# Kernel optimization log

Measured on AMD Instinct MI355X. Metric: run time of the kernel, lower is better.

## Reference

```python
import jax, jax.numpy as jnp
import numpy as np

D_MODEL = 1024
N_HEADS = 16
HEAD_DIM = D_MODEL // N_HEADS
WINDOW = 256


def setup_inputs() -> dict:
    key = jax.random.key(0)
    kx, kq, ko = jax.random.split(key, 3)
    B, T = 4, 2048
    x = jax.random.normal(kx, (B, T, D_MODEL), dtype=jnp.float32)
    s = 1.0 / np.sqrt(D_MODEL)
    w_qkv = jax.random.normal(kq, (D_MODEL, 3 * D_MODEL), dtype=jnp.float32) * s
    w_out = jax.random.normal(ko, (D_MODEL, D_MODEL), dtype=jnp.float32) * s
    return {"x": x, "w_qkv": w_qkv, "w_out": w_out}


def reference(x, w_qkv, w_out):
    B, T, C = x.shape
    qkv = (x @ w_qkv).reshape(B, T, 3, N_HEADS, HEAD_DIM)
    q, k, v = qkv[:, :, 0], qkv[:, :, 1], qkv[:, :, 2]  # [B,T,H,D]
    # sliding-window causal mask: position i attends to j in (i-W, i]
    i = jnp.arange(T)[:, None]
    j = jnp.arange(T)[None, :]
    allowed = (j <= i) & (j > i - WINDOW)
    mask = jnp.where(allowed, 0.0, -jnp.inf).astype(x.dtype)  # [T,T]
    scale = 1.0 / np.sqrt(HEAD_DIM)
    scores = jnp.einsum('bqhd,bkhd->bhqk', q, k) * scale + mask
    attn = jax.nn.softmax(scores, axis=-1)
    out = jnp.einsum('bhqk,bkhd->bqhd', attn, v).reshape(B, T, C)
    return out @ w_out
```

## Files before the change

### kernel.cpp

```cpp
#include <hip/hip_runtime.h>

typedef unsigned short u16;
typedef __attribute__((ext_vector_type(8))) short bh8;
typedef __attribute__((ext_vector_type(4))) float f4;
typedef __attribute__((ext_vector_type(4))) unsigned short us4;

#define T_SEQ 2048
#define NHEADS 16
#define DHEAD 64
#define WIN 256

__device__ __forceinline__ float bf2f(u16 u) {
  union { unsigned int i; float f; } v; v.i = ((unsigned int)u) << 16; return v.f;
}
__device__ __forceinline__ u16 f2bf(float f) {
  unsigned int u = __float_as_uint(f);
  u = u + 0x7fffu + ((u >> 16) & 1u);
  return (u16)(u >> 16);
}
__device__ __forceinline__ void async16(const void* g, void* l) {
  void* gv = const_cast<void*>(g);
  __builtin_amdgcn_global_load_lds(
      (__attribute__((address_space(1))) void*)gv,
      (__attribute__((address_space(3))) void*)l, 16, 0, 0);
}

__global__ void detect_dtype(const void* x, int* flag) {
  if (threadIdx.x == 0 && blockIdx.x == 0) {
    const float* xf = (const float*)x;
    int ok = 1;
    for (int i = 0; i < 128; ++i) {
      float v = xf[i];
      float a = fabsf(v);
      if (!(a < 64.f)) { ok = 0; break; }
      if (!(v == 0.f || a > 1e-30f)) { ok = 0; break; }
    }
    *flag = ok;
  }
}

__global__ __launch_bounds__(256) void prep(
    const void* __restrict__ x, const void* __restrict__ w_qkv,
    const void* __restrict__ w_out, u16* __restrict__ xbf,
    u16* __restrict__ wqkvT, u16* __restrict__ woutT,
    const int* __restrict__ flag, int have_x)
{
  const int bid = blockIdx.x;
  const int tid = threadIdx.x;
  const int isf = *flag;

  if (bid < 4096) {
    if (!have_x) return;
    const size_t e = ((size_t)bid * 256 + tid) * 8;
    if (isf) {
      const float* f = (const float*)x;
      us4 o0, o1;
      #pragma unroll
      for (int u = 0; u < 4; ++u) { o0[u] = f2bf(f[e + u]); o1[u] = f2bf(f[e + 4 + u]); }
      *(us4*)&xbf[e] = o0; *(us4*)&xbf[e + 4] = o1;
    } else {
      *(us4*)&xbf[e]     = *(const us4*)&((const u16*)x)[e];
      *(us4*)&xbf[e + 4] = *(const us4*)&((const u16*)x)[e + 4];
    }
  } else {
    __shared__ alignas(16) u16 tile[32][33];
    const void* in; u16* out; int C, bx, by;
    if (bid < 4096 + 3072) { const int t = bid - 4096; in = w_qkv; out = wqkvT; C = 3072; bx = t % 96; by = t / 96; }
    else                   { const int t = bid - 7168; in = w_out; out = woutT; C = 1024; bx = t % 32; by = t / 32; }
    const int R = 1024;
    const int tx = tid & 31, ty = tid >> 5;
    const int xg = bx * 32 + tx;
    const int y0 = by * 32;
    #pragma unroll
    for (int i = ty; i < 32; i += 8) {
      u16 v;
      if (isf) v = f2bf(((const float*)in)[(size_t)(y0 + i) * C + xg]);
      else     v = ((const u16*)in)[(size_t)(y0 + i) * C + xg];
      tile[i][tx] = v;
    }
    __syncthreads();
    const int ox  = y0 + tx;
    const int oy0 = bx * 32;
    #pragma unroll
    for (int i = ty; i < 32; i += 8)
      out[(size_t)(oy0 + i) * R + ox] = tile[tx][i];
  }
}

template<bool ADYN, bool CDYN>
__global__ __launch_bounds__(256, 4) void gemm_bt(
    const void* __restrict__ A, const u16* __restrict__ Bt,
    void* __restrict__ C, int N, int K, int lda, int ldc,
    const int* __restrict__ flag)
{
  __shared__ alignas(16) u16 As[128 * 64];
  __shared__ alignas(16) u16 Bs[128 * 64];

  const int isf  = ADYN ? *flag : 0;
  const int tid  = threadIdx.x;
  const int lane = tid & 63;
  const int w    = tid >> 6;
  const int wm   = (w >> 1) * 64;
  const int wn   = (w & 1) * 64;
  const int quad = lane >> 4;
  const int l16  = lane & 15;
  const int row0 = blockIdx.y * 128;
  const int col0 = blockIdx.x * 128;

  f4 acc[4][4] = {};

  size_t aoff[4]; const u16* bsrc[4]; int lofs[4];
  #pragma unroll
  for (int s = 0; s < 4; ++s) {
    const int r  = s * 32 + (tid >> 3);
    const int gc = (tid & 7) ^ (r & 7);
    aoff[s] = (size_t)(row0 + r) * lda + gc * 8;
    bsrc[s] = Bt + (size_t)(col0 + r) * K + gc * 8;
    lofs[s] = s * 4096 + tid * 16;
  }

  const bool af32 = ADYN && isf;

  for (int k0 = 0; k0 < K; k0 += 64) {
    if (af32) {
      const float* Af = (const float*)A;
      bh8 a[4];
      #pragma unroll
      for (int s = 0; s < 4; ++s) {
        f4 u0 = *(const f4*)(Af + aoff[s] + k0);
        f4 u1 = *(const f4*)(Af + aoff[s] + k0 + 4);
        #pragma unroll
        for (int u = 0; u < 4; ++u) { a[s][u] = (short)f2bf(u0[u]); a[s][u + 4] = (short)f2bf(u1[u]); }
      }
      __syncthreads();
      #pragma unroll
      for (int s = 0; s < 4; ++s) {
        *(bh8*)((char*)As + lofs[s]) = a[s];
        async16(bsrc[s] + k0, (char*)Bs + lofs[s]);
      }
    } else {
      const u16* A16 = (const u16*)A;
      __syncthreads();
      #pragma unroll
      for (int s = 0; s < 4; ++s) {
        async16(A16 + aoff[s] + k0, (char*)As + lofs[s]);
        async16(bsrc[s] + k0,       (char*)Bs + lofs[s]);
      }
    }
    __builtin_amdgcn_s_waitcnt(0);
    __syncthreads();

    #pragma unroll
    for (int ks = 0; ks < 2; ++ks) {
      bh8 af[4], bf[4];
      #pragma unroll
      for (int i = 0; i < 4; ++i) {
        const int row = wm + i * 16 + l16;
        const int lc  = (ks * 4 + quad) ^ (row & 7);
        af[i] = *(const bh8*)(As + row * 64 + lc * 8);
      }
      #pragma unroll
      for (int j = 0; j < 4; ++j) {
        const int row = wn + j * 16 + l16;
        const int lc  = (ks * 4 + quad) ^ (row & 7);
        bf[j] = *(const bh8*)(Bs + row * 64 + lc * 8);
      }
      #pragma unroll
      for (int i = 0; i < 4; ++i)
        #pragma unroll
        for (int j = 0; j < 4; ++j)
          acc[i][j] = __builtin_amdgcn_mfma_f32_16x16x32_bf16(af[i], bf[j], acc[i][j], 0, 0, 0);
    }
  }

  const bool cf32 = CDYN && (*flag);
  #pragma unroll
  for (int i = 0; i < 4; ++i) {
    #pragma unroll
    for (int j = 0; j < 4; ++j) {
      const int rb = row0 + wm + i * 16 + quad * 4;
      const int cc = col0 + wn + j * 16 + l16;
      #pragma unroll
      for (int r = 0; r < 4; ++r) {
        if (cf32) ((float*)C)[(size_t)(rb + r) * ldc + cc] = acc[i][j][r];
        else      ((u16*)C)[(size_t)(rb + r) * ldc + cc]   = f2bf(acc[i][j][r]);
      }
    }
  }
}

__global__ __launch_bounds__(256) void attn_mfma(u16* __restrict__ qkv)
{
  __shared__ alignas(16) u16 Qs[64 * 72];
  __shared__ alignas(16) u16 Kt[64 * 72];
  __shared__ alignas(16) u16 Vt[64 * 72];
  __shared__ alignas(16) u16 Ps[64 * 72];

  const int tid  = threadIdx.x;
  const int lane = tid & 63;
  const int w    = tid >> 6;
  const int quad = lane >> 4;
  const int l16  = lane & 15;
  const int qb = blockIdx.x, h = blockIdx.y, b = blockIdx.z;
  const int qs = qb * 64;

  const u16* base = qkv + (size_t)b * T_SEQ * 3072 + h * 64;

  const int c8  = (tid & 7) * 8;
  const int r0s = tid >> 3;
  #pragma unroll
  for (int r = r0s; r < 64; r += 32)
    *(bh8*)&Qs[r * 72 + c8] = *(const bh8*)&base[(size_t)(qs + r) * 3072 + c8];

  f4 Oc[4] = {};
  float mst[4] = {-1e30f, -1e30f, -1e30f, -1e30f};
  float lst[4] = {0.f, 0.f, 0.f, 0.f};

  const int tmin = (qb >= 4) ? 0 : (4 - qb);

  for (int t = tmin; t < 5; ++t) {
    const int kt0 = qs - 256 + t * 64;
    __syncthreads();

    #pragma unroll
    for (int r = r0s; r < 64; r += 32) {
      *(bh8*)&Kt[r * 72 + c8] =
          *(const bh8*)&base[(size_t)(kt0 + r) * 3072 + 1024 + c8];
      bh8 v = *(const bh8*)&base[(size_t)(kt0 + r) * 3072 + 2048 + c8];
      const int kc = r >> 3, ki = r & 7;
      #pragma unroll
      for (int u = 0; u < 8; ++u) {
        const int d = c8 + u;
        Vt[d * 72 + ((kc ^ (d >> 3)) << 3) + ki] = (u16)v[u];
      }
    }
    __syncthreads();

    const int qrow = (w * 16 + l16) * 72;
    bh8 qa0 = *(const bh8*)&Qs[qrow + quad * 8];
    bh8 qa1 = *(const bh8*)&Qs[qrow + 32 + quad * 8];
    f4 S[4];
    #pragma unroll
    for (int kb = 0; kb < 4; ++kb) {
      const int krow = (kb * 16 + l16) * 72;
      bh8 kf0 = *(const bh8*)&Kt[krow + quad * 8];
      bh8 kf1 = *(const bh8*)&Kt[krow + 32 + quad * 8];
      f4 s = {};
      s = __builtin_amdgcn_mfma_f32_16x16x32_bf16(qa0, kf0, s, 0, 0, 0);
      s = __builtin_amdgcn_mfma_f32_16x16x32_bf16(qa1, kf1, s, 0, 0, 0);
      S[kb] = s;
    }

    const int iq0 = qs + w * 16 + quad * 4;
    float tmax[4] = {-1e30f, -1e30f, -1e30f, -1e30f};
    #pragma unroll
    for (int kb = 0; kb < 4; ++kb) {
      const int j = kt0 + kb * 16 + l16;
      #pragma unroll
      for (int rr = 0; rr < 4; ++rr) {
        const int i = iq0 + rr;
        float s = S[kb][rr] * 0.125f;
        const bool ok = (j <= i) && (j > i - WIN);
        s = ok ? s : -1e30f;
        S[kb][rr] = s;
        tmax[rr] = fmaxf(tmax[rr], s);
      }
    }
    #pragma unroll
    for (int off = 1; off < 16; off <<= 1)
      #pragma unroll
      for (int rr = 0; rr < 4; ++rr)
        tmax[rr] = fmaxf(tmax[rr], __shfl_xor(tmax[rr], off));

    float alpha[4], rsum[4];
    #pragma unroll
    for (int rr = 0; rr < 4; ++rr) {
      const float mnew = fmaxf(mst[rr], tmax[rr]);
      alpha[rr] = __expf(mst[rr] - mnew);
      mst[rr] = mnew;
      rsum[rr] = 0.f;
    }

    const int swq = quad >> 1;
    #pragma unroll
    for (int kb = 0; kb < 4; ++kb) {
      const int kc = kb * 2 + (l16 >> 3);
      const int ki = l16 & 7;
      #pragma unroll
      for (int rr = 0; rr < 4; ++rr) {
        const float sv = S[kb][rr];
        const float p = (sv > -0.5e30f) ? __expf(sv - mst[rr]) : 0.f;
        rsum[rr] += p;
        const int q = w * 16 + quad * 4 + rr;
        Ps[q * 72 + ((kc ^ swq) << 3) + ki] = f2bf(p);
      }
    }
    #pragma unroll
    for (int off = 1; off < 16; off <<= 1)
      #pragma unroll
      for (int rr = 0; rr < 4; ++rr)
        rsum[rr] += __shfl_xor(rsum[rr], off);
    #pragma unroll
    for (int rr = 0; rr < 4; ++rr)
      lst[rr] = lst[rr] * alpha[rr] + rsum[rr];

    #pragma unroll
    for (int db = 0; db < 4; ++db)
      #pragma unroll
      for (int rr = 0; rr < 4; ++rr)
        Oc[db][rr] *= alpha[rr];

    {
      const int q = w * 16 + l16;
      const int sw = (q >> 3) & 1;
      bh8 pa0 = *(const bh8*)&Ps[q * 72 + (((0 + quad) ^ sw) << 3)];
      bh8 pa1 = *(const bh8*)&Ps[q * 72 + (((4 + quad) ^ sw) << 3)];
      #pragma unroll
      for (int db = 0; db < 4; ++db) {
        const int d = db * 16 + l16;
        const int dsw = d >> 3;
        bh8 vb0 = *(const bh8*)&Vt[d * 72 + (((0 + quad) ^ dsw) << 3)];
        bh8 vb1 = *(const bh8*)&Vt[d * 72 + (((4 + quad) ^ dsw) << 3)];
        Oc[db] = __builtin_amdgcn_mfma_f32_16x16x32_bf16(pa0, vb0, Oc[db], 0, 0, 0);
        Oc[db] = __builtin_amdgcn_mfma_f32_16x16x32_bf16(pa1, vb1, Oc[db], 0, 0, 0);
      }
    }
  }

  u16* obase = (u16*)base;
  #pragma unroll
  for (int rr = 0; rr < 4; ++rr) {
    const int i = qs + w * 16 + quad * 4 + rr;
    const float inv = 1.f / lst[rr];
    #pragma unroll
    for (int db = 0; db < 4; ++db)
      obase[(size_t)i * 3072 + db * 16 + l16] = f2bf(Oc[db][rr] * inv);
  }
}

extern "C" void kernel_launch(void* const* d_in, const int* in_sizes, int n_in,
                              void* d_out, int out_size, void* d_ws, size_t ws_size,
                              hipStream_t stream) {
  const void* x     = d_in[0];
  const void* w_qkv = d_in[1];
  const void* w_out = d_in[2];

  const size_t SZ_QKV  = (size_t)8192 * 3072 * 2;
  const size_t SZ_XBF  = (size_t)8192 * 1024 * 2;
  const size_t SZ_WQ   = (size_t)3072 * 1024 * 2;
  const size_t SZ_WO   = (size_t)1024 * 1024 * 2;

  char* p = (char*)d_ws;
  u16* qkv   = (u16*)p; p += SZ_QKV;
  u16* wqkvT = (u16*)p; p += SZ_WQ;
  u16* woutT = (u16*)p; p += SZ_WO;
  int* flag  = (int*)p; p += 16;
  u16* xbf   = (u16*)p;
  const bool have_x = ws_size >= (SZ_QKV + SZ_WQ + SZ_WO + 16 + SZ_XBF);

  detect_dtype<<<1, 64, 0, stream>>>(x, flag);

  prep<<<dim3(8192), 256, 0, stream>>>(x, w_qkv, w_out, xbf, wqkvT, woutT,
                                       flag, have_x ? 1 : 0);

  if (have_x) {
    gemm_bt<false, false><<<dim3(24, 64), 256, 0, stream>>>(
        xbf, wqkvT, qkv, 3072, 1024, 1024, 3072, flag);
  } else {
    gemm_bt<true, false><<<dim3(24, 64), 256, 0, stream>>>(
        x, wqkvT, qkv, 3072, 1024, 1024, 3072, flag);
  }

  attn_mfma<<<dim3(32, NHEADS, 4), 256, 0, stream>>>(qkv);

  gemm_bt<false, true><<<dim3(8, 64), 256, 0, stream>>>(
      qkv, woutT, d_out, 1024, 1024, 3072, 1024, flag);
}
```

Measured before the change: 239.3 us.

## Narrow output GEMM tile, load Q to registers, parallelize dtype detection

Adds a column-tile template parameter to the bf16 GEMM and runs the output projection with 64-wide tiles, doubling its grid from 512 to 1024 blocks so more CUs stay busy. The attention kernel now loads Q fragments straight from global memory into registers instead of staging them through shared memory. The dtype-detection kernel uses 256 threads with a wave vote in place of a serial single-thread loop. The narrower tile gives less reuse of each A tile per block and more A traffic in exchange for better occupancy.

```diff
diff --git a/kernel.cpp b/kernel.cpp
--- a/kernel.cpp
+++ b/kernel.cpp
@@ -26,17 +26,15 @@
 }
 
 __global__ void detect_dtype(const void* x, int* flag) {
-  if (threadIdx.x == 0 && blockIdx.x == 0) {
-    const float* xf = (const float*)x;
-    int ok = 1;
-    for (int i = 0; i < 128; ++i) {
-      float v = xf[i];
-      float a = fabsf(v);
-      if (!(a < 64.f)) { ok = 0; break; }
-      if (!(v == 0.f || a > 1e-30f)) { ok = 0; break; }
-    }
-    *flag = ok;
-  }
+  __shared__ int bad;
+  if (threadIdx.x == 0) bad = 0;
+  __syncthreads();
+  const float v = ((const float*)x)[threadIdx.x];
+  const float a = fabsf(v);
+  const int lane_bad = (!(a < 64.f)) || (!(v == 0.f || a > 1e-30f));
+  if (__any(lane_bad)) { if ((threadIdx.x & 63) == 0) bad = 1; }
+  __syncthreads();
+  if (threadIdx.x == 0) *flag = bad ? 0 : 1;
 }
 
 __global__ __launch_bounds__(256) void prep(
@@ -87,36 +85,43 @@
   }
 }
 
-template<bool ADYN, bool CDYN>
+template<bool ADYN, bool CDYN, int BN>
 __global__ __launch_bounds__(256, 4) void gemm_bt(
     const void* __restrict__ A, const u16* __restrict__ Bt,
     void* __restrict__ C, int N, int K, int lda, int ldc,
     const int* __restrict__ flag)
 {
+  constexpr int NJ = BN / 32;
+  constexpr int SB = BN / 32;
   __shared__ alignas(16) u16 As[128 * 64];
-  __shared__ alignas(16) u16 Bs[128 * 64];
+  __shared__ alignas(16) u16 Bs[BN * 64];
 
   const int isf  = ADYN ? *flag : 0;
   const int tid  = threadIdx.x;
   const int lane = tid & 63;
   const int w    = tid >> 6;
   const int wm   = (w >> 1) * 64;
-  const int wn   = (w & 1) * 64;
+  const int wn   = (w & 1) * (BN / 2);
   const int quad = lane >> 4;
   const int l16  = lane & 15;
   const int row0 = blockIdx.y * 128;
-  const int col0 = blockIdx.x * 128;
-
-  f4 acc[4][4] = {};
-
-  size_t aoff[4]; const u16* bsrc[4]; int lofs[4];
+  const int col0 = blockIdx.x * BN;
+
+  f4 acc[4][NJ] = {};
+
+  size_t aoff[4]; const u16* bsrc[SB]; int lofs[4];
   #pragma unroll
   for (int s = 0; s < 4; ++s) {
     const int r  = s * 32 + (tid >> 3);
     const int gc = (tid & 7) ^ (r & 7);
     aoff[s] = (size_t)(row0 + r) * lda + gc * 8;
+    lofs[s] = s * 4096 + tid * 16;
+  }
+  #pragma unroll
+  for (int s = 0; s < SB; ++s) {
+    const int r  = s * 32 + (tid >> 3);
+    const int gc = (tid & 7) ^ (r & 7);
     bsrc[s] = Bt + (size_t)(col0 + r) * K + gc * 8;
-    lofs[s] = s * 4096 + tid * 16;
   }
 
   const bool af32 = ADYN && isf;
@@ -134,25 +139,23 @@
       }
       __syncthreads();
       #pragma unroll
-      for (int s = 0; s < 4; ++s) {
-        *(bh8*)((char*)As + lofs[s]) = a[s];
-        async16(bsrc[s] + k0, (char*)Bs + lofs[s]);
-      }
+      for (int s = 0; s < 4; ++s) *(bh8*)((char*)As + lofs[s]) = a[s];
+      #pragma unroll
+      for (int s = 0; s < SB; ++s) async16(bsrc[s] + k0, (char*)Bs + lofs[s]);
     } else {
       const u16* A16 = (const u16*)A;
       __syncthreads();
       #pragma unroll
-      for (int s = 0; s < 4; ++s) {
-        async16(A16 + aoff[s] + k0, (char*)As + lofs[s]);
-        async16(bsrc[s] + k0,       (char*)Bs + lofs[s]);
-      }
+      for (int s = 0; s < 4; ++s) async16(A16 + aoff[s] + k0, (char*)As + lofs[s]);
+      #pragma unroll
+      for (int s = 0; s < SB; ++s) async16(bsrc[s] + k0, (char*)Bs + lofs[s]);
     }
     __builtin_amdgcn_s_waitcnt(0);
     __syncthreads();
 
     #pragma unroll
     for (int ks = 0; ks < 2; ++ks) {
-      bh8 af[4], bf[4];
+      bh8 af[4], bf[NJ];
       #pragma unroll
       for (int i = 0; i < 4; ++i) {
         const int row = wm + i * 16 + l16;
@@ -160,7 +163,7 @@
         af[i] = *(const bh8*)(As + row * 64 + lc * 8);
       }
       #pragma unroll
-      for (int j = 0; j < 4; ++j) {
+      for (int j = 0; j < NJ; ++j) {
         const int row = wn + j * 16 + l16;
         const int lc  = (ks * 4 + quad) ^ (row & 7);
         bf[j] = *(const bh8*)(Bs + row * 64 + lc * 8);
@@ -168,7 +171,7 @@
       #pragma unroll
       for (int i = 0; i < 4; ++i)
         #pragma unroll
-        for (int j = 0; j < 4; ++j)
+        for (int j = 0; j < NJ; ++j)
           acc[i][j] = __builtin_amdgcn_mfma_f32_16x16x32_bf16(af[i], bf[j], acc[i][j], 0, 0, 0);
     }
   }
@@ -177,7 +180,7 @@
   #pragma unroll
   for (int i = 0; i < 4; ++i) {
     #pragma unroll
-    for (int j = 0; j < 4; ++j) {
+    for (int j = 0; j < NJ; ++j) {
       const int rb = row0 + wm + i * 16 + quad * 4;
       const int cc = col0 + wn + j * 16 + l16;
       #pragma unroll
@@ -191,7 +194,6 @@
 
 __global__ __launch_bounds__(256) void attn_mfma(u16* __restrict__ qkv)
 {
-  __shared__ alignas(16) u16 Qs[64 * 72];
   __shared__ alignas(16) u16 Kt[64 * 72];
   __shared__ alignas(16) u16 Vt[64 * 72];
   __shared__ alignas(16) u16 Ps[64 * 72];
@@ -206,17 +208,17 @@
 
   const u16* base = qkv + (size_t)b * T_SEQ * 3072 + h * 64;
 
-  const int c8  = (tid & 7) * 8;
-  const int r0s = tid >> 3;
-  #pragma unroll
-  for (int r = r0s; r < 64; r += 32)
-    *(bh8*)&Qs[r * 72 + c8] = *(const bh8*)&base[(size_t)(qs + r) * 3072 + c8];
+  const size_t qrowg = (size_t)(qs + w * 16 + l16) * 3072;
+  bh8 qa0 = *(const bh8*)&base[qrowg + quad * 8];
+  bh8 qa1 = *(const bh8*)&base[qrowg + 32 + quad * 8];
 
   f4 Oc[4] = {};
   float mst[4] = {-1e30f, -1e30f, -1e30f, -1e30f};
   float lst[4] = {0.f, 0.f, 0.f, 0.f};
 
   const int tmin = (qb >= 4) ? 0 : (4 - qb);
+  const int c8  = (tid & 7) * 8;
+  const int r0s = tid >> 3;
 
   for (int t = tmin; t < 5; ++t) {
     const int kt0 = qs - 256 + t * 64;
@@ -236,9 +238,6 @@
     }
     __syncthreads();
 
-    const int qrow = (w * 16 + l16) * 72;
-    bh8 qa0 = *(const bh8*)&Qs[qrow + quad * 8];
-    bh8 qa1 = *(const bh8*)&Qs[qrow + 32 + quad * 8];
     f4 S[4];
     #pragma unroll
     for (int kb = 0; kb < 4; ++kb) {
@@ -358,21 +357,21 @@
   u16* xbf   = (u16*)p;
   const bool have_x = ws_size >= (SZ_QKV + SZ_WQ + SZ_WO + 16 + SZ_XBF);
 
-  detect_dtype<<<1, 64, 0, stream>>>(x, flag);
+  detect_dtype<<<1, 256, 0, stream>>>(x, flag);
 
   prep<<<dim3(8192), 256, 0, stream>>>(x, w_qkv, w_out, xbf, wqkvT, woutT,
                                        flag, have_x ? 1 : 0);
 
   if (have_x) {
-    gemm_bt<false, false><<<dim3(24, 64), 256, 0, stream>>>(
+    gemm_bt<false, false, 128><<<dim3(24, 64), 256, 0, stream>>>(
         xbf, wqkvT, qkv, 3072, 1024, 1024, 3072, flag);
   } else {
-    gemm_bt<true, false><<<dim3(24, 64), 256, 0, stream>>>(
+    gemm_bt<true, false, 128><<<dim3(24, 64), 256, 0, stream>>>(
         x, wqkvT, qkv, 3072, 1024, 1024, 3072, flag);
   }
 
   attn_mfma<<<dim3(32, NHEADS, 4), 256, 0, stream>>>(qkv);
 
-  gemm_bt<false, true><<<dim3(8, 64), 256, 0, stream>>>(
+  gemm_bt<false, true, 64><<<dim3(16, 64), 256, 0, stream>>>(
       qkv, woutT, d_out, 1024, 1024, 3072, 1024, flag);
 }
```

Result: faster. 225.3 us (-5.8%).
